# Kernel optimization log

Measured on AMD Instinct MI355X. Metric: run time of the kernel, lower is better.

## Reference

```python
import jax, jax.numpy as jnp
import numpy as np

N_NODES = 50000
N_EDGES = 800000
DIM = 64
N_ETYPES = 4
N_STEPS = 5


def setup_inputs() -> dict:
    key = jax.random.key(0)
    ks = jax.random.split(key, 10)
    feat = jax.random.normal(ks[0], (N_NODES, DIM), dtype=jnp.float32)
    src = jax.random.randint(ks[1], (N_EDGES,), 0, N_NODES, dtype=jnp.int32)
    dst = jax.random.randint(ks[2], (N_EDGES,), 0, N_NODES, dtype=jnp.int32)
    etypes = jax.random.randint(ks[3], (N_EDGES,), 0, N_ETYPES, dtype=jnp.int32)
    # per-edge-type Linear weights, xavier_normal with relu gain, zero bias
    gain = float(np.sqrt(2.0))
    std = gain * float(np.sqrt(2.0 / (DIM + DIM)))
    W = jax.random.normal(ks[4], (N_ETYPES, DIM, DIM), dtype=jnp.float32) * std  # [T, out, in]
    b = jnp.zeros((N_ETYPES, DIM), dtype=jnp.float32)
    # GRUCell params (torch layout: [3*dim, dim], gates order r,z,n), uniform(-1/sqrt(dim), 1/sqrt(dim))
    bound = 1.0 / float(np.sqrt(DIM))
    w_ih = jax.random.uniform(ks[5], (3 * DIM, DIM), minval=-bound, maxval=bound, dtype=jnp.float32)
    w_hh = jax.random.uniform(ks[6], (3 * DIM, DIM), minval=-bound, maxval=bound, dtype=jnp.float32)
    b_ih = jax.random.uniform(ks[7], (3 * DIM,), minval=-bound, maxval=bound, dtype=jnp.float32)
    b_hh = jax.random.uniform(ks[8], (3 * DIM,), minval=-bound, maxval=bound, dtype=jnp.float32)
    return {"feat": feat, "W": W, "b": b, "w_ih": w_ih, "w_hh": w_hh,
            "b_ih": b_ih, "b_hh": b_hh, "src": src, "dst": dst, "etypes": etypes}


def _gru_cell(a, h, w_ih, w_hh, b_ih, b_hh):
    gi = a @ w_ih.T + b_ih  # [N, 3*D]
    gh = h @ w_hh.T + b_hh
    i_r, i_z, i_n = jnp.split(gi, 3, axis=-1)
    h_r, h_z, h_n = jnp.split(gh, 3, axis=-1)
    r = jax.nn.sigmoid(i_r + h_r)
    z = jax.nn.sigmoid(i_z + h_z)
    n = jnp.tanh(i_n + r * h_n)
    return (1.0 - z) * n + z * h


def reference(feat, W, b, w_ih, w_hh, b_ih, b_hh, src, dst, etypes):
    n_nodes = feat.shape[0]
    h = feat
    for _ in range(N_STEPS):
        # apply every etype linear to all nodes: [N, T, D]
        h_all = jnp.einsum('nd,ted->nte', h, W) + b
        # per-edge message selects src node under its edge type: [E, D]
        m = h_all[src, etypes]
        # scatter-sum to destination nodes: [N, D]
        a = jax.ops.segment_sum(m, dst, num_segments=n_nodes)
        h = _gru_cell(a, h, w_ih, w_hh, b_ih, b_hh)
    return h
```

## Files before the change

kernel.cpp:

```cpp
#include <hip/hip_runtime.h>
#include <hip/hip_bf16.h>
#include <cstdint>

#define DIM 64
#define NSTEPS 5
#define HS  68
#define GLDH 194
#define ATS 292
#define MAXVDEG 32

typedef __attribute__((ext_vector_type(8))) short short8v;
typedef __attribute__((ext_vector_type(4))) float f32x4;
typedef __attribute__((ext_vector_type(8))) _Float16 half8v;

__device__ __forceinline__ float sigmoidf_(float x){ return 1.0f/(1.0f+expf(-x)); }

__device__ __forceinline__ unsigned short f2bf(float x){
  unsigned u = __builtin_bit_cast(unsigned, x);
  return (unsigned short)((u + 0x7FFFu + ((u>>16)&1u)) >> 16);
}
__device__ __forceinline__ float bf2f(unsigned short b){
  unsigned u = ((unsigned)b)<<16;
  return __builtin_bit_cast(float, u);
}

__device__ __forceinline__ void splitbf8(const float* __restrict__ p,
                                         short8v& hi, short8v& lo){
  float4 x0 = *(const float4*)p;
  float4 x1 = *(const float4*)(p+4);
  float xs[8] = {x0.x,x0.y,x0.z,x0.w,x1.x,x1.y,x1.z,x1.w};
#pragma unroll
  for(int i=0;i<8;i++){
    unsigned short hb = f2bf(xs[i]);
    float rem = xs[i] - bf2f(hb);
    hi[i] = (short)hb;
    lo[i] = (short)f2bf(rem);
  }
}

__global__ __launch_bounds__(256) void k_pack(const float* __restrict__ src,
    short* __restrict__ ph, short* __restrict__ pl, int ncoltiles){
  int idx = blockIdx.x*256 + threadIdx.x;
  int total = ncoltiles*1024;
  if (idx >= total) return;
  int e = idx & 7, lane = (idx>>3)&63, kc = (idx>>9)&1, ct = idx>>10;
  int col = ct*16 + (lane&15);
  int k = kc*32 + (lane>>4)*8 + e;
  float v = src[(size_t)col*DIM + k];
  unsigned short hb = f2bf(v);
  ph[idx] = (short)hb;
  pl[idx] = (short)f2bf(v - bf2f(hb));
}

__global__ __launch_bounds__(256) void k_pack256(const float* __restrict__ W,
    const float* __restrict__ b, short* __restrict__ ph, short* __restrict__ pl){
  int idx = blockIdx.x*256 + threadIdx.x;
  if (idx >= 4*9*512) return;
  int e = idx & 7, lane = (idx>>3)&63, r = idx>>9;
  int kc = r % 9, ct = r / 9;
  int col = ct*16 + (lane&15);
  int k = kc*32 + (lane>>4)*8 + e;
  float v = 0.0f;
  if (k < 256){ int t = k>>6, d = k&63; v = W[(size_t)(t*64+col)*DIM + d]; }
  else if (k < 260){ v = b[(size_t)(k-256)*DIM + col]; }
  unsigned short hb = f2bf(v);
  ph[idx] = (short)hb;
  pl[idx] = (short)f2bf(v - bf2f(hb));
}

__global__ __launch_bounds__(256) void k_cast(const float* __restrict__ x,
                                              _Float16* __restrict__ y, int n4){
  int i = blockIdx.x*256 + threadIdx.x;
  if (i >= n4) return;
  float4 v = *(const float4*)(x + (size_t)i*4);
  y[(size_t)i*4+0] = (_Float16)v.x; y[(size_t)i*4+1] = (_Float16)v.y;
  y[(size_t)i*4+2] = (_Float16)v.z; y[(size_t)i*4+3] = (_Float16)v.w;
}

__global__ __launch_bounds__(256) void k_scatter_vell(
    const int* __restrict__ src, const int* __restrict__ dst,
    const int* __restrict__ et, int* __restrict__ deg4,
    int* __restrict__ ell, int n_edges) {
  int e = blockIdx.x * 256 + threadIdx.x;
  if (e >= n_edges) return;
  int vn = dst[e]*4 + et[e];
  int rank = atomicAdd(&deg4[vn], 1);
  if (rank < MAXVDEG)
    ell[(size_t)vn * MAXVDEG + rank] = src[e];
}

__global__ __launch_bounds__(256) void k_step(
    const _Float16* __restrict__ hb_in, _Float16* __restrict__ hb_out,
    const int* __restrict__ ell, const int* __restrict__ deg4,
    float* __restrict__ h,
    const short* __restrict__ pw_h, const short* __restrict__ pw_l,
    const short* __restrict__ pih_h, const short* __restrict__ pih_l,
    const short* __restrict__ phh_h, const short* __restrict__ phh_l,
    const float* __restrict__ b_ih, const float* __restrict__ b_hh,
    int n_nodes, int write_hb){
  __shared__ __align__(16) char smem[16*ATS*4 + 16*HS*4];
  float (*atile)[ATS] = (float(*)[ATS])smem;
  _Float16* gbuf      = (_Float16*)smem;
  float (*abuf)[HS]   = (float(*)[HS])(smem + 16*ATS*4);

  const int tid = threadIdx.x;
  const int wave = tid >> 6, lane = tid & 63;
  const int n0 = blockIdx.x * 16;
  if (n0 >= n_nodes) return;

  {
    int vl = tid >> 2;
    int q  = tid & 3;
    int jn = vl >> 2;
    int t  = vl & 3;
    int vng = (n0 << 2) + vl;
    int dg = min(deg4[vng], MAXVDEG);
    const int* ebase = ell + (size_t)vng * MAXVDEG;
    float acc[16];
#pragma unroll
    for (int k=0;k<16;k++) acc[k]=0.0f;
    int i = 0;
    for (; i + 1 < dg; i += 2) {
      int s0 = ebase[i], s1 = ebase[i+1];
      half8v a0 = *(const half8v*)(hb_in + (size_t)s0*DIM + q*16);
      half8v a1 = *(const half8v*)(hb_in + (size_t)s0*DIM + q*16 + 8);
      half8v c0 = *(const half8v*)(hb_in + (size_t)s1*DIM + q*16);
      half8v c1 = *(const half8v*)(hb_in + (size_t)s1*DIM + q*16 + 8);
#pragma unroll
      for (int k=0;k<8;k++){ acc[k]   += (float)a0[k] + (float)c0[k];
                             acc[8+k] += (float)a1[k] + (float)c1[k]; }
    }
    if (i < dg) {
      int s0 = ebase[i];
      half8v a0 = *(const half8v*)(hb_in + (size_t)s0*DIM + q*16);
      half8v a1 = *(const half8v*)(hb_in + (size_t)s0*DIM + q*16 + 8);
#pragma unroll
      for (int k=0;k<8;k++){ acc[k] += (float)a0[k]; acc[8+k] += (float)a1[k]; }
    }
    float* dstp = &atile[jn][t*64 + q*16];
#pragma unroll
    for (int w=0;w<4;w++){
      float4 v = {acc[w*4+0],acc[w*4+1],acc[w*4+2],acc[w*4+3]};
      *(float4*)(dstp + w*4) = v;
    }
    if (q == 0) atile[jn][256 + t] = (float)dg;
    int zr = tid >> 4, zc = 260 + (tid & 15);
    atile[zr][zc] = 0.0f;
    atile[zr][zc + 16] = 0.0f;
  }
  __syncthreads();

  const int rr = (lane >> 4) * 4;
  const int cc = lane & 15;
  {
    const float* arow = &atile[lane & 15][0];
    const int koff = (lane >> 4) * 8;
    f32x4 acc4 = {0.f,0.f,0.f,0.f};
#pragma unroll
    for (int kc = 0; kc < 9; ++kc){
      short8v ah, al;
      splitbf8(arow + kc*32 + koff, ah, al);
      const short8v bh = *(const short8v*)(pw_h + ((size_t)(wave*9+kc)*64 + lane)*8);
      const short8v bl = *(const short8v*)(pw_l + ((size_t)(wave*9+kc)*64 + lane)*8);
      acc4 = __builtin_amdgcn_mfma_f32_16x16x32_bf16(ah, bl, acc4, 0,0,0);
      acc4 = __builtin_amdgcn_mfma_f32_16x16x32_bf16(al, bh, acc4, 0,0,0);
      acc4 = __builtin_amdgcn_mfma_f32_16x16x32_bf16(ah, bh, acc4, 0,0,0);
    }
    __syncthreads();
#pragma unroll
    for (int q=0;q<4;q++) abuf[rr+q][wave*16 + cc] = acc4[q];
  }
  __syncthreads();

  const bool is_h = wave >= 2;
  const short* __restrict__ pbh = is_h ? phh_h : pih_h;
  const short* __restrict__ pbl = is_h ? phh_l : pih_l;
  const float* __restrict__ bv  = is_h ? b_hh : b_ih;
  _Float16* outb = gbuf + (is_h ? 16*GLDH : 0);

  const int kb = (lane >> 4) * 8;
  short8v ah0,al0,ah1,al1;
  if (is_h) {
    const float* xp = h + (size_t)(n0 + (lane & 15))*DIM;
    splitbf8(xp + kb,      ah0, al0);
    splitbf8(xp + 32 + kb, ah1, al1);
  } else {
    const float* xp = &abuf[lane & 15][0];
    splitbf8(xp + kb,      ah0, al0);
    splitbf8(xp + 32 + kb, ah1, al1);
  }

  const int ct0 = (wave & 1) * 6;
#pragma unroll
  for (int i = 0; i < 6; ++i){
    int ct = ct0 + i;
    const short8v bh0 = *(const short8v*)(pbh + ((size_t)(ct*2+0)*64 + lane)*8);
    const short8v bh1 = *(const short8v*)(pbh + ((size_t)(ct*2+1)*64 + lane)*8);
    const short8v bl0 = *(const short8v*)(pbl + ((size_t)(ct*2+0)*64 + lane)*8);
    const short8v bl1 = *(const short8v*)(pbl + ((size_t)(ct*2+1)*64 + lane)*8);
    float bias = bv[ct*16 + cc];
    f32x4 acc = {bias,bias,bias,bias};
    acc = __builtin_amdgcn_mfma_f32_16x16x32_bf16(ah0, bh0, acc, 0,0,0);
    acc = __builtin_amdgcn_mfma_f32_16x16x32_bf16(ah1, bh1, acc, 0,0,0);
    acc = __builtin_amdgcn_mfma_f32_16x16x32_bf16(al0, bh0, acc, 0,0,0);
    acc = __builtin_amdgcn_mfma_f32_16x16x32_bf16(al1, bh1, acc, 0,0,0);
    acc = __builtin_amdgcn_mfma_f32_16x16x32_bf16(ah0, bl0, acc, 0,0,0);
    acc = __builtin_amdgcn_mfma_f32_16x16x32_bf16(ah1, bl1, acc, 0,0,0);
#pragma unroll
    for (int q=0;q<4;q++)
      outb[(rr+q)*GLDH + ct*16 + cc] = (_Float16)acc[q];
  }
  __syncthreads();

#pragma unroll
  for (int it=0; it<4; ++it){
    int t = it*256 + tid;
    int j = t >> 6, d = t & 63;
    float gir = (float)gbuf[j*GLDH + d];
    float giz = (float)gbuf[j*GLDH + 64 + d];
    float gin = (float)gbuf[j*GLDH + 128 + d];
    float ghr = (float)gbuf[16*GLDH + j*GLDH + d];
    float ghz = (float)gbuf[16*GLDH + j*GLDH + 64 + d];
    float ghn = (float)gbuf[16*GLDH + j*GLDH + 128 + d];
    float r  = sigmoidf_(gir + ghr);
    float z  = sigmoidf_(giz + ghz);
    float nv = tanhf    (gin + r*ghn);
    size_t off = (size_t)(n0+j)*DIM + d;
    float ho = h[off];
    float hn = (1.0f - z)*nv + z*ho;
    h[off] = hn;
    if (write_hb) hb_out[off] = (_Float16)hn;
  }
}

extern "C" void kernel_launch(void* const* d_in, const int* in_sizes, int n_in,
                              void* d_out, int out_size, void* d_ws, size_t ws_size,
                              hipStream_t stream) {
  const float* feat = (const float*)d_in[0];
  const float* W    = (const float*)d_in[1];
  const float* b    = (const float*)d_in[2];
  const float* w_ih = (const float*)d_in[3];
  const float* w_hh = (const float*)d_in[4];
  const float* b_ih = (const float*)d_in[5];
  const float* b_hh = (const float*)d_in[6];
  const int* src = (const int*)d_in[7];
  const int* dst = (const int*)d_in[8];
  const int* et  = (const int*)d_in[9];

  const int n_nodes = in_sizes[0] / DIM;
  const int n_edges = in_sizes[7];

  float* h = (float*)d_out;
  char* ws = (char*)d_ws;
  _Float16* hb0 = (_Float16*)ws;  ws += (size_t)n_nodes * DIM * sizeof(_Float16);
  _Float16* hb1 = (_Float16*)ws;  ws += (size_t)n_nodes * DIM * sizeof(_Float16);
  int* ell  = (int*)ws;   ws += (size_t)n_nodes * 4 * MAXVDEG * sizeof(int);
  int* deg4 = (int*)ws;   ws += (size_t)n_nodes * 4 * sizeof(int);
  short* pw_h  = (short*)ws;  ws += 18432 * sizeof(short);
  short* pw_l  = (short*)ws;  ws += 18432 * sizeof(short);
  short* pih_h = (short*)ws;  ws += 12288 * sizeof(short);
  short* pih_l = (short*)ws;  ws += 12288 * sizeof(short);
  short* phh_h = (short*)ws;  ws += 12288 * sizeof(short);
  short* phh_l = (short*)ws;  ws += 12288 * sizeof(short);

  hipMemcpyAsync(h, feat, (size_t)n_nodes * DIM * sizeof(float),
                 hipMemcpyDeviceToDevice, stream);

  k_pack256<<<72, 256, 0, stream>>>(W, b, pw_h, pw_l);
  k_pack<<<48, 256, 0, stream>>>(w_ih, pih_h, pih_l, 12);
  k_pack<<<48, 256, 0, stream>>>(w_hh, phh_h, phh_l, 12);
  k_cast<<<(n_nodes*DIM/4 + 255)/256, 256, 0, stream>>>(feat, hb0, n_nodes*DIM/4);

  const int nblk_edges = (n_edges + 255) / 256;
  hipMemsetAsync(deg4, 0, (size_t)n_nodes * 4 * sizeof(int), stream);
  k_scatter_vell<<<nblk_edges, 256, 0, stream>>>(src, dst, et, deg4, ell, n_edges);

  const int rtiles = (n_nodes + 15) / 16;

  for (int s = 0; s < NSTEPS; ++s) {
    const _Float16* hin = (s & 1) ? hb1 : hb0;
    _Float16* hout      = (s & 1) ? hb0 : hb1;
    k_step<<<rtiles, 256, 0, stream>>>(hin, hout, ell, deg4, h,
                                       pw_h, pw_l, pih_h, pih_l, phh_h, phh_l,
                                       b_ih, b_hh, n_nodes,
                                       (s < NSTEPS - 1) ? 1 : 0);
  }
}
```

Baseline: 323.6 us.

## Split neighbor gather into separate kernel and switch W GEMM to fp16 split-weight MFMA

Moves the per-(node, edge type) neighbor aggregation out of the fused step kernel into its own k_gather kernel. It uses 8 threads per virtual node and vectorized int4 index loads, and writes fp16 aggregated sums plus degrees to a global staging buffer. The step kernel then loads that tile and runs the typed-linear GEMM with fp16 MFMA: one fp16 A operand against hi/lo fp16 weights, two MFMAs per k-chunk instead of three bf16 ones. The goal is more parallelism and latency hiding for the random gathers and cheaper MFMA work. The costs are an extra global round trip of the staging buffer each step, an extra launch per step, lower precision from storing aggregated sums in fp16, and a smaller per-vnode degree cap of 28.

```diff
diff --git a/kernel.cpp b/kernel.cpp
--- a/kernel.cpp
+++ b/kernel.cpp
@@ -6,8 +6,8 @@
 #define NSTEPS 5
 #define HS  68
 #define GLDH 194
-#define ATS 292
-#define MAXVDEG 32
+#define SW  288
+#define MAXVDEG 28
 
 typedef __attribute__((ext_vector_type(8))) short short8v;
 typedef __attribute__((ext_vector_type(4))) float f32x4;
@@ -53,7 +53,7 @@
 }
 
 __global__ __launch_bounds__(256) void k_pack256(const float* __restrict__ W,
-    const float* __restrict__ b, short* __restrict__ ph, short* __restrict__ pl){
+    const float* __restrict__ b, _Float16* __restrict__ ph, _Float16* __restrict__ pl){
   int idx = blockIdx.x*256 + threadIdx.x;
   if (idx >= 4*9*512) return;
   int e = idx & 7, lane = (idx>>3)&63, r = idx>>9;
@@ -63,9 +63,9 @@
   float v = 0.0f;
   if (k < 256){ int t = k>>6, d = k&63; v = W[(size_t)(t*64+col)*DIM + d]; }
   else if (k < 260){ v = b[(size_t)(k-256)*DIM + col]; }
-  unsigned short hb = f2bf(v);
-  ph[idx] = (short)hb;
-  pl[idx] = (short)f2bf(v - bf2f(hb));
+  _Float16 hv = (_Float16)v;
+  ph[idx] = hv;
+  pl[idx] = (_Float16)(v - (float)hv);
 }
 
 __global__ __launch_bounds__(256) void k_cast(const float* __restrict__ x,
@@ -89,82 +89,76 @@
     ell[(size_t)vn * MAXVDEG + rank] = src[e];
 }
 
+__global__ __launch_bounds__(256) void k_gather(
+    const _Float16* __restrict__ hb, const int* __restrict__ ell,
+    const int* __restrict__ deg4, _Float16* __restrict__ s, int n_vnodes){
+  int gid = blockIdx.x*256 + threadIdx.x;
+  int vn = gid >> 3;
+  if (vn >= n_vnodes) return;
+  int q = gid & 7;
+  int dg = min(deg4[vn], MAXVDEG);
+  const int* ebase = ell + (size_t)vn * MAXVDEG;
+  float acc[8] = {0,0,0,0,0,0,0,0};
+  int i = 0;
+  for (; i + 3 < dg; i += 4) {
+    int4 p = *(const int4*)(ebase + i);
+    half8v v0 = *(const half8v*)(hb + (size_t)p.x*DIM + q*8);
+    half8v v1 = *(const half8v*)(hb + (size_t)p.y*DIM + q*8);
+    half8v v2 = *(const half8v*)(hb + (size_t)p.z*DIM + q*8);
+    half8v v3 = *(const half8v*)(hb + (size_t)p.w*DIM + q*8);
+#pragma unroll
+    for (int k=0;k<8;k++)
+      acc[k] += ((float)v0[k] + (float)v1[k]) + ((float)v2[k] + (float)v3[k]);
+  }
+  for (; i < dg; ++i) {
+    int sx = ebase[i];
+    half8v v0 = *(const half8v*)(hb + (size_t)sx*DIM + q*8);
+#pragma unroll
+    for (int k=0;k<8;k++) acc[k] += (float)v0[k];
+  }
+  int n = vn >> 2, t = vn & 3;
+  half8v out;
+#pragma unroll
+  for (int k=0;k<8;k++) out[k] = (_Float16)acc[k];
+  *(half8v*)(s + (size_t)n*SW + t*DIM + q*8) = out;
+  if (q == 0) s[(size_t)n*SW + 256 + t] = (_Float16)dg;
+}
+
 __global__ __launch_bounds__(256) void k_step(
-    const _Float16* __restrict__ hb_in, _Float16* __restrict__ hb_out,
-    const int* __restrict__ ell, const int* __restrict__ deg4,
+    const _Float16* __restrict__ s, _Float16* __restrict__ hb,
     float* __restrict__ h,
-    const short* __restrict__ pw_h, const short* __restrict__ pw_l,
+    const _Float16* __restrict__ pw_h, const _Float16* __restrict__ pw_l,
     const short* __restrict__ pih_h, const short* __restrict__ pih_l,
     const short* __restrict__ phh_h, const short* __restrict__ phh_l,
     const float* __restrict__ b_ih, const float* __restrict__ b_hh,
     int n_nodes, int write_hb){
-  __shared__ __align__(16) char smem[16*ATS*4 + 16*HS*4];
-  float (*atile)[ATS] = (float(*)[ATS])smem;
-  _Float16* gbuf      = (_Float16*)smem;
-  float (*abuf)[HS]   = (float(*)[HS])(smem + 16*ATS*4);
+  __shared__ __align__(16) char smem[12416 + 4352];
+  _Float16* stile = (_Float16*)smem;
+  _Float16* gbuf  = (_Float16*)smem;
+  float (*abuf)[HS] = (float(*)[HS])(smem + 12416);
 
   const int tid = threadIdx.x;
   const int wave = tid >> 6, lane = tid & 63;
   const int n0 = blockIdx.x * 16;
   if (n0 >= n_nodes) return;
 
-  {
-    int vl = tid >> 2;
-    int q  = tid & 3;
-    int jn = vl >> 2;
-    int t  = vl & 3;
-    int vng = (n0 << 2) + vl;
-    int dg = min(deg4[vng], MAXVDEG);
-    const int* ebase = ell + (size_t)vng * MAXVDEG;
-    float acc[16];
-#pragma unroll
-    for (int k=0;k<16;k++) acc[k]=0.0f;
-    int i = 0;
-    for (; i + 1 < dg; i += 2) {
-      int s0 = ebase[i], s1 = ebase[i+1];
-      half8v a0 = *(const half8v*)(hb_in + (size_t)s0*DIM + q*16);
-      half8v a1 = *(const half8v*)(hb_in + (size_t)s0*DIM + q*16 + 8);
-      half8v c0 = *(const half8v*)(hb_in + (size_t)s1*DIM + q*16);
-      half8v c1 = *(const half8v*)(hb_in + (size_t)s1*DIM + q*16 + 8);
-#pragma unroll
-      for (int k=0;k<8;k++){ acc[k]   += (float)a0[k] + (float)c0[k];
-                             acc[8+k] += (float)a1[k] + (float)c1[k]; }
-    }
-    if (i < dg) {
-      int s0 = ebase[i];
-      half8v a0 = *(const half8v*)(hb_in + (size_t)s0*DIM + q*16);
-      half8v a1 = *(const half8v*)(hb_in + (size_t)s0*DIM + q*16 + 8);
-#pragma unroll
-      for (int k=0;k<8;k++){ acc[k] += (float)a0[k]; acc[8+k] += (float)a1[k]; }
-    }
-    float* dstp = &atile[jn][t*64 + q*16];
-#pragma unroll
-    for (int w=0;w<4;w++){
-      float4 v = {acc[w*4+0],acc[w*4+1],acc[w*4+2],acc[w*4+3]};
-      *(float4*)(dstp + w*4) = v;
-    }
-    if (q == 0) atile[jn][256 + t] = (float)dg;
-    int zr = tid >> 4, zc = 260 + (tid & 15);
-    atile[zr][zc] = 0.0f;
-    atile[zr][zc + 16] = 0.0f;
-  }
+  for (int t = tid; t < 576; t += 256)
+    *(half8v*)(stile + t*8) = *(const half8v*)(s + (size_t)n0*SW + t*8);
   __syncthreads();
 
   const int rr = (lane >> 4) * 4;
   const int cc = lane & 15;
   {
-    const float* arow = &atile[lane & 15][0];
     const int koff = (lane >> 4) * 8;
+    const int arow = lane & 15;
     f32x4 acc4 = {0.f,0.f,0.f,0.f};
 #pragma unroll
     for (int kc = 0; kc < 9; ++kc){
-      short8v ah, al;
-      splitbf8(arow + kc*32 + koff, ah, al);
-      const short8v bh = *(const short8v*)(pw_h + ((size_t)(wave*9+kc)*64 + lane)*8);
-      const short8v bl = *(const short8v*)(pw_l + ((size_t)(wave*9+kc)*64 + lane)*8);
-      acc4 = __builtin_amdgcn_mfma_f32_16x16x32_bf16(ah, bl, acc4, 0,0,0);
-      acc4 = __builtin_amdgcn_mfma_f32_16x16x32_bf16(al, bh, acc4, 0,0,0);
-      acc4 = __builtin_amdgcn_mfma_f32_16x16x32_bf16(ah, bh, acc4, 0,0,0);
+      half8v ah = *(const half8v*)(stile + arow*SW + kc*32 + koff);
+      const half8v bh = *(const half8v*)(pw_h + ((size_t)(wave*9+kc)*64 + lane)*8);
+      const half8v bl = *(const half8v*)(pw_l + ((size_t)(wave*9+kc)*64 + lane)*8);
+      acc4 = __builtin_amdgcn_mfma_f32_16x16x32_f16(ah, bh, acc4, 0,0,0);
+      acc4 = __builtin_amdgcn_mfma_f32_16x16x32_f16(ah, bl, acc4, 0,0,0);
     }
     __syncthreads();
 #pragma unroll
@@ -229,7 +223,7 @@
     float ho = h[off];
     float hn = (1.0f - z)*nv + z*ho;
     h[off] = hn;
-    if (write_hb) hb_out[off] = (_Float16)hn;
+    if (write_hb) hb[off] = (_Float16)hn;
   }
 }
 
@@ -249,15 +243,16 @@
 
   const int n_nodes = in_sizes[0] / DIM;
   const int n_edges = in_sizes[7];
+  const int n_vnodes = n_nodes * 4;
 
   float* h = (float*)d_out;
   char* ws = (char*)d_ws;
-  _Float16* hb0 = (_Float16*)ws;  ws += (size_t)n_nodes * DIM * sizeof(_Float16);
-  _Float16* hb1 = (_Float16*)ws;  ws += (size_t)n_nodes * DIM * sizeof(_Float16);
-  int* ell  = (int*)ws;   ws += (size_t)n_nodes * 4 * MAXVDEG * sizeof(int);
-  int* deg4 = (int*)ws;   ws += (size_t)n_nodes * 4 * sizeof(int);
-  short* pw_h  = (short*)ws;  ws += 18432 * sizeof(short);
-  short* pw_l  = (short*)ws;  ws += 18432 * sizeof(short);
+  _Float16* hb = (_Float16*)ws;  ws += (size_t)n_nodes * DIM * sizeof(_Float16);
+  _Float16* s  = (_Float16*)ws;  ws += (size_t)n_nodes * SW * sizeof(_Float16);
+  int* ell  = (int*)ws;   ws += (size_t)n_vnodes * MAXVDEG * sizeof(int);
+  int* deg4 = (int*)ws;   ws += (size_t)n_vnodes * sizeof(int);
+  _Float16* pw_h = (_Float16*)ws;  ws += 18432 * sizeof(_Float16);
+  _Float16* pw_l = (_Float16*)ws;  ws += 18432 * sizeof(_Float16);
   short* pih_h = (short*)ws;  ws += 12288 * sizeof(short);
   short* pih_l = (short*)ws;  ws += 12288 * sizeof(short);
   short* phh_h = (short*)ws;  ws += 12288 * sizeof(short);
@@ -269,20 +264,21 @@
   k_pack256<<<72, 256, 0, stream>>>(W, b, pw_h, pw_l);
   k_pack<<<48, 256, 0, stream>>>(w_ih, pih_h, pih_l, 12);
   k_pack<<<48, 256, 0, stream>>>(w_hh, phh_h, phh_l, 12);
-  k_cast<<<(n_nodes*DIM/4 + 255)/256, 256, 0, stream>>>(feat, hb0, n_nodes*DIM/4);
+  k_cast<<<(n_nodes*DIM/4 + 255)/256, 256, 0, stream>>>(feat, hb, n_nodes*DIM/4);
+  hipMemsetAsync(s, 0, (size_t)n_nodes * SW * sizeof(_Float16), stream);
 
   const int nblk_edges = (n_edges + 255) / 256;
-  hipMemsetAsync(deg4, 0, (size_t)n_nodes * 4 * sizeof(int), stream);
+  hipMemsetAsync(deg4, 0, (size_t)n_vnodes * sizeof(int), stream);
   k_scatter_vell<<<nblk_edges, 256, 0, stream>>>(src, dst, et, deg4, ell, n_edges);
 
+  const int ggrid  = (n_vnodes * 8 + 255) / 256;
   const int rtiles = (n_nodes + 15) / 16;
 
-  for (int s = 0; s < NSTEPS; ++s) {
-    const _Float16* hin = (s & 1) ? hb1 : hb0;
-    _Float16* hout      = (s & 1) ? hb0 : hb1;
-    k_step<<<rtiles, 256, 0, stream>>>(hin, hout, ell, deg4, h,
+  for (int st = 0; st < NSTEPS; ++st) {
+    k_gather<<<ggrid, 256, 0, stream>>>(hb, ell, deg4, s, n_vnodes);
+    k_step<<<rtiles, 256, 0, stream>>>(s, hb, h,
                                        pw_h, pw_l, pih_h, pih_l, phh_h, phh_l,
                                        b_ih, b_hh, n_nodes,
-                                       (s < NSTEPS - 1) ? 1 : 0);
-  }
-}
+                                       (st < NSTEPS - 1) ? 1 : 0);
+  }
+}
```

Result: slower. 344.3 us (+6.4%).
